# Kernel optimization log

Hardware: AMD Instinct MI355X
Metric: run time of the kernel (lower is better)

The kernel has to match this reference:

```python
import jax, jax.numpy as jnp
import numpy as np
from jax import lax

B, N, C, T = 8, 2000, 32, 12
K, F_CHEV, F_TIME = 3, 64, 64
LN_EPS = 1e-5


def setup_inputs() -> dict:
    key = jax.random.key(0)
    ks = jax.random.split(key, 20)
    s = 0.1
    return {
        "x": jax.random.normal(ks[0], (B, N, C, T), jnp.float32),
        "cheb_polys": jax.random.normal(ks[1], (K, N, N), jnp.float32) * 0.02,
        # temporal attention params
        "U1": jax.random.normal(ks[2], (N,), jnp.float32) * s,
        "U2": jax.random.normal(ks[3], (C, N), jnp.float32) * s,
        "U3": jax.random.normal(ks[4], (C,), jnp.float32) * s,
        "be": jax.random.normal(ks[5], (1, T, T), jnp.float32) * s,
        "Ve": jax.random.normal(ks[6], (T, T), jnp.float32) * s,
        # spatial attention params
        "W1": jax.random.normal(ks[7], (T,), jnp.float32) * s,
        "W2": jax.random.normal(ks[8], (C, T), jnp.float32) * s,
        "W3": jax.random.normal(ks[9], (C,), jnp.float32) * s,
        "bs": jax.random.normal(ks[10], (1, N, N), jnp.float32) * s,
        "Vs": jax.random.normal(ks[11], (N, N), jnp.float32) * (s / np.sqrt(N)),
        # Chebyshev conv params, stacked (K, C, F_chev)
        "Theta": jax.random.normal(ks[12], (K, C, F_CHEV), jnp.float32) * (1.0 / np.sqrt(C)),
        # time conv (1x3) and residual conv (1x1), NCHW/OIHW layout
        "tc_w": jax.random.normal(ks[13], (F_TIME, F_CHEV, 1, 3), jnp.float32) * (1.0 / np.sqrt(3 * F_CHEV)),
        "tc_b": jnp.zeros((F_TIME,), jnp.float32),
        "rc_w": jax.random.normal(ks[14], (F_TIME, C, 1, 1), jnp.float32) * (1.0 / np.sqrt(C)),
        "rc_b": jnp.zeros((F_TIME,), jnp.float32),
        # LayerNorm over nb_time_filter
        "ln_g": jnp.ones((F_TIME,), jnp.float32),
        "ln_b": jnp.zeros((F_TIME,), jnp.float32),
    }


def _conv2d(x, w, b, stride_t):
    # x: (B, Cin, N, T), w: (Cout, Cin, kh, kw)
    pad_w = (w.shape[3] - 1) // 2
    y = lax.conv_general_dilated(
        x, w, window_strides=(1, stride_t),
        padding=[(0, 0), (pad_w, pad_w)],
        dimension_numbers=("NCHW", "OIHW", "NCHW"))
    return y + b[None, :, None, None]


def reference(x, cheb_polys, U1, U2, U3, be, Ve, W1, W2, W3, bs, Vs,
              Theta, tc_w, tc_b, rc_w, rc_b, ln_g, ln_b):
    b, n, c, t = x.shape

    # ---- temporal attention: (B, T, T) ----
    lhs = jnp.einsum("bnct,n->btc", x, U1)              # x.permute(0,3,2,1) @ U1
    lhs = jnp.einsum("btc,cn->btn", lhs, U2)
    rhs = jnp.einsum("c,bnct->bnt", U3, x)
    E = jnp.einsum("ij,bjk->bik", Ve,
                   jax.nn.sigmoid(jnp.einsum("btn,bnu->btu", lhs, rhs) + be))
    temporal_At = jax.nn.softmax(E, axis=1)             # (B, T, T)

    # apply temporal attention
    x_TAt = jnp.matmul(x.reshape(b, n * c, t), temporal_At).reshape(b, n, c, t)

    # ---- spatial attention on x_TAt: (B, N, N) ----
    lhs_s = jnp.einsum("bnct,t->bnc", x_TAt, W1)
    lhs_s = jnp.einsum("bnc,ct->bnt", lhs_s, W2)
    rhs_s = jnp.einsum("c,bnct->btn", W3, x_TAt)        # (W3 @ x).transpose(-1,-2)
    S = jnp.einsum("ij,bjk->bik", Vs,
                   jax.nn.sigmoid(jnp.einsum("bnt,btm->bnm", lhs_s, rhs_s) + bs))
    spatial_At = jax.nn.softmax(S, axis=1)              # (B, N, N)

    # ---- Chebyshev graph conv with spatial attention ----
    # A[b,k,j,i] = cheb[k,j,i] * SAt[b,j,i]; out = relu(sum_k A^T x Theta_k)
    A = cheb_polys[None, :, :, :] * spatial_At[:, None, :, :]   # (B, K, N, N)
    h = jnp.einsum("bkji,bjct->bkitc", A, x)                    # (B, K, N, T, C)
    spatial_gcn = jax.nn.relu(jnp.einsum("bkitc,kcf->bift", h, Theta))  # (B, N, F, T)

    # ---- temporal conv + residual + LayerNorm ----
    time_out = _conv2d(spatial_gcn.transpose(0, 2, 1, 3), tc_w, tc_b, 1)  # (B, F_time, N, T')
    x_res = _conv2d(x.transpose(0, 2, 1, 3), rc_w, rc_b, 1)               # (B, F_time, N, T')
    z = jax.nn.relu(x_res + time_out).transpose(0, 3, 2, 1)               # (B, T', N, F_time)

    mu = jnp.mean(z, axis=-1, keepdims=True)
    var = jnp.mean((z - mu) ** 2, axis=-1, keepdims=True)
    zn = (z - mu) * lax.rsqrt(var + LN_EPS) * ln_g + ln_b

    return zn.transpose(0, 2, 3, 1)                                       # (B, N, F_time, T')
```

## Files before the change

### kernel.cpp

```cpp
#include <hip/hip_runtime.h>
#include <hip/hip_bf16.h>
#include <math.h>

#define B_ 8
#define N_ 2000
#define C_ 32
#define T_ 12
#define K_ 3
#define FC_ 64
#define FT_ 64
#define PW 2048

typedef short bf16x8 __attribute__((ext_vector_type(8)));
typedef float f32x4 __attribute__((ext_vector_type(4)));

__device__ __forceinline__ float sigmoidf(float v) { return 1.0f / (1.0f + __expf(-v)); }
__device__ __forceinline__ float bf2f(unsigned short u) {
    union { unsigned int i; float f; } v; v.i = ((unsigned int)u) << 16; return v.f;
}
__device__ __forceinline__ unsigned short f2bf(float f) {
    union { __hip_bfloat16 h; unsigned short u; } v; v.h = __float2bfloat16(f); return v.u;
}
typedef const __attribute__((address_space(1))) void* gas_t;
typedef __attribute__((address_space(3))) void* las_t;
__device__ __forceinline__ void gload16(const unsigned short* g, unsigned short* l) {
    __builtin_amdgcn_global_load_lds((gas_t)g, (las_t)l, 16, 0, 0);
}

__global__ __launch_bounds__(256) void k_tprep(const float* __restrict__ x, const float* __restrict__ U1,
                                               const float* __restrict__ U3,
                                               float* __restrict__ rhsT, float* __restrict__ plh) {
    int b = blockIdx.y, chunk = blockIdx.x;
    int tid = threadIdx.x;
    int nl = tid >> 5, c = tid & 31;
    int w = tid >> 6;
    float u3 = U3[c];
    float plA[12];
#pragma unroll
    for (int t = 0; t < 12; ++t) plA[t] = 0.f;
    for (int it = 0; it < 5; ++it) {
        int n = chunk * 40 + it * 8 + nl;
        const float* xp = x + ((size_t)(b * 2000 + n) * 32 + c) * 12;
        float4 v0 = *(const float4*)xp, v1 = *(const float4*)(xp + 4), v2 = *(const float4*)(xp + 8);
        float xv[12] = {v0.x, v0.y, v0.z, v0.w, v1.x, v1.y, v1.z, v1.w, v2.x, v2.y, v2.z, v2.w};
        float rv[12];
#pragma unroll
        for (int t = 0; t < 12; ++t) rv[t] = u3 * xv[t];
#pragma unroll
        for (int off = 16; off >= 1; off >>= 1)
#pragma unroll
            for (int t = 0; t < 12; ++t) rv[t] += __shfl_xor(rv[t], off);
        if (c == 0) {
#pragma unroll
            for (int t = 0; t < 12; ++t) rhsT[(size_t)(b * 2000 + n) * 12 + t] = rv[t];
        }
        float u1 = U1[n];
#pragma unroll
        for (int t = 0; t < 12; ++t) plA[t] += u1 * xv[t];
    }
#pragma unroll
    for (int t = 0; t < 12; ++t) plA[t] += __shfl_xor(plA[t], 32);
    __shared__ float accs[4][32][12];
    if ((tid & 63) < 32) {
#pragma unroll
        for (int t = 0; t < 12; ++t) accs[w][c][t] = plA[t];
    }
    __syncthreads();
    if (tid < 384) {
        int c2 = tid / 12, t2 = tid % 12;
        float s = accs[0][c2][t2] + accs[1][c2][t2] + accs[2][c2][t2] + accs[3][c2][t2];
        plh[((size_t)(b * 50 + chunk)) * 384 + tid] = s;
    }
}

__global__ __launch_bounds__(256) void k_tred(const float* __restrict__ plh, float* __restrict__ lhs1) {
    int b = blockIdx.x;
    for (int q = threadIdx.x; q < 384; q += 256) {
        const float* p = plh + (size_t)b * 50 * 384 + q;
        float s = 0.f;
        for (int ch = 0; ch < 50; ++ch) s += p[(size_t)ch * 384];
        int c = q / 12, t = q % 12;
        lhs1[(b * 12 + t) * 32 + c] = s;
    }
}

__global__ __launch_bounds__(256) void k_lhsT(const float* __restrict__ lhs1, const float* __restrict__ U2,
                                              float* __restrict__ lhsT) {
    int gid = blockIdx.x * 256 + threadIdx.x;
    if (gid >= B_ * T_ * N_) return;
    int n = gid % N_;
    int bt = gid / N_;
    const float* l1 = lhs1 + bt * C_;
    float a = 0.f;
#pragma unroll
    for (int c = 0; c < C_; ++c) a += l1[c] * U2[c * N_ + n];
    lhsT[gid] = a;
}

__global__ __launch_bounds__(256) void k_tatt1(const float* __restrict__ lhsT, const float* __restrict__ rhsT,
                                               float* __restrict__ pP) {
    int b = blockIdx.y, ch = blockIdx.x;
    int tid = threadIdx.x;
    int n0 = ch * 125;
    __shared__ float sL[12][128];
    __shared__ float sR[128][12];
    for (int q = tid; q < 12 * 125; q += 256) {
        int t = q / 125, nn = q % 125;
        sL[t][nn] = lhsT[(size_t)(b * 12 + t) * 2000 + n0 + nn];
    }
    for (int q = tid; q < 125 * 12; q += 256) {
        int nn = q / 12, t = q % 12;
        sR[nn][t] = rhsT[(size_t)(b * 2000 + n0 + nn) * 12 + t];
    }
    __syncthreads();
    if (tid < 144) {
        int tP = tid / 12, uP = tid % 12;
        float a = 0.f;
#pragma unroll 5
        for (int nn = 0; nn < 125; ++nn) a += sL[tP][nn] * sR[nn][uP];
        pP[(size_t)(b * 16 + ch) * 144 + tid] = a;
    }
}

__global__ __launch_bounds__(256) void k_tatt2(const float* __restrict__ pP, const float* __restrict__ be,
                                               const float* __restrict__ Ve, float* __restrict__ At) {
    int b = blockIdx.x, tid = threadIdx.x;
    __shared__ float sp[144], sE[144], mk[12], sk[12];
    int tP = tid / 12, uP = tid % 12;
    if (tid < 144) {
        float a = 0.f;
#pragma unroll
        for (int ch = 0; ch < 16; ++ch) a += pP[(size_t)(b * 16 + ch) * 144 + tid];
        sp[tid] = sigmoidf(a + be[tid]);
    }
    __syncthreads();
    if (tid < 144) {
        float e = 0.f;
#pragma unroll
        for (int j = 0; j < 12; ++j) e += Ve[tP * 12 + j] * sp[j * 12 + uP];
        sE[tid] = e;
    }
    __syncthreads();
    if (tid < 12) {
        float m = -1e30f;
#pragma unroll
        for (int i = 0; i < 12; ++i) m = fmaxf(m, sE[i * 12 + tid]);
        float s = 0.f;
#pragma unroll
        for (int i = 0; i < 12; ++i) s += __expf(sE[i * 12 + tid] - m);
        mk[tid] = m; sk[tid] = 1.0f / s;
    }
    __syncthreads();
    if (tid < 144) At[b * 144 + tid] = __expf(sE[tid] - mk[uP]) * sk[uP];
}

__global__ __launch_bounds__(256) void k_xsp(const float* __restrict__ x, const float* __restrict__ At,
                                             const float* __restrict__ W1, const float* __restrict__ W2,
                                             const float* __restrict__ W3,
                                             float* __restrict__ lhs_s, float* __restrict__ rhs_s) {
    int b = blockIdx.y, chunk = blockIdx.x;
    int tid = threadIdx.x, nl = tid >> 5, c = tid & 31;
    int n = chunk * 8 + nl;
    __shared__ float atl[144];
    __shared__ float w2l[384];
    __shared__ float w1l[12];
    if (tid < 144) atl[tid] = At[b * 144 + tid];
    if (tid >= 144 && tid < 156) w1l[tid - 144] = W1[tid - 144];
    for (int q = tid; q < 384; q += 256) w2l[q] = W2[q];
    __syncthreads();
    const float* xp = x + ((size_t)(b * 2000 + n) * 32 + c) * 12;
    float4 v0 = *(const float4*)xp, v1 = *(const float4*)(xp + 4), v2 = *(const float4*)(xp + 8);
    float xv[12] = {v0.x, v0.y, v0.z, v0.w, v1.x, v1.y, v1.z, v1.w, v2.x, v2.y, v2.z, v2.w};
    float xa[12];
#pragma unroll
    for (int t = 0; t < 12; ++t) {
        float s = 0.f;
#pragma unroll
        for (int u = 0; u < 12; ++u) s += xv[u] * atl[u * 12 + t];
        xa[t] = s;
    }
    float w3 = W3[c];
    float rv[12], lv[12];
    float l1 = 0.f;
#pragma unroll
    for (int t = 0; t < 12; ++t) l1 += xa[t] * w1l[t];
#pragma unroll
    for (int t = 0; t < 12; ++t) { rv[t] = w3 * xa[t]; lv[t] = l1 * w2l[c * 12 + t]; }
#pragma unroll
    for (int off = 16; off >= 1; off >>= 1)
#pragma unroll
        for (int t = 0; t < 12; ++t) { rv[t] += __shfl_xor(rv[t], off); lv[t] += __shfl_xor(lv[t], off); }
    if (c == 0) {
#pragma unroll
        for (int t = 0; t < 12; ++t) rhs_s[(size_t)(b * 12 + t) * 2000 + n] = rv[t];
#pragma unroll
        for (int t = 0; t < 12; ++t) lhs_s[(size_t)(b * 2000 + n) * 12 + t] = lv[t];
    }
}

__global__ __launch_bounds__(256) void k_wprep(const float* __restrict__ tc_w, const float* __restrict__ rc_w,
                                               float* __restrict__ tcwT, float* __restrict__ rcwT) {
    int gid = blockIdx.x * 256 + threadIdx.x;
    if (gid < 12288) {
        int fi = gid / 192, rem = gid % 192, f = rem / 3, d = rem % 3;
        tcwT[gid] = tc_w[(f * 64 + fi) * 3 + d];
    } else if (gid < 14336) {
        int q = gid - 12288;
        int c = q >> 6, f = q & 63;
        rcwT[q] = rc_w[f * 32 + c];
    }
}

__global__ __launch_bounds__(256) void k_vsb(const float* __restrict__ Vs, unsigned short* __restrict__ Vsb) {
    int gid = blockIdx.x * 256 + threadIdx.x;
    int row = gid >> 8, chunk = gid & 255;
    int p0 = chunk * 8;
    unsigned short o[8];
#pragma unroll
    for (int e = 0; e < 8; ++e) {
        int p = p0 + e;
        o[e] = (row < N_ && p < N_) ? f2bf(Vs[row * N_ + p]) : (unsigned short)0;
    }
    *(int4*)(Vsb + (size_t)row * PW + p0) = *(int4*)o;
}

__global__ __launch_bounds__(256) void k_chebT(const float* __restrict__ cheb, unsigned short* __restrict__ chebT) {
    int j0 = blockIdx.x * 64, i0 = blockIdx.y * 64, kk = blockIdx.z;
    __shared__ float Tl[64][65];
    int t = threadIdx.x;
    int rr = t >> 2, c0 = (t & 3) * 16;
    int j = j0 + rr;
#pragma unroll
    for (int e = 0; e < 16; ++e) {
        int i = i0 + c0 + e;
        Tl[rr][c0 + e] = (j < N_ && i < N_) ? cheb[(size_t)kk * 4000000 + (size_t)j * N_ + i] : 0.f;
    }
    __syncthreads();
    int l = t & 63, w = t >> 6;
    unsigned short o[16];
#pragma unroll
    for (int e = 0; e < 16; ++e) o[e] = f2bf(Tl[w * 16 + e][l]);
    unsigned short* dst = chebT + (size_t)kk * PW * PW + (size_t)(i0 + l) * PW + j0 + w * 16;
    *(int4*)dst = *(int4*)o;
    *(int4*)(dst + 8) = *(int4*)(o + 8);
}

__global__ __launch_bounds__(256) void k_xT(const float* __restrict__ x, unsigned short* __restrict__ xT) {
    int j0 = blockIdx.x * 64, r0 = blockIdx.y * 64, b = blockIdx.z;
    __shared__ float Tl[64][65];
    int t = threadIdx.x;
    int rr = t >> 2, c0 = (t & 3) * 16;
    int j = j0 + rr;
#pragma unroll
    for (int e = 0; e < 16; ++e) {
        int r = r0 + c0 + e;
        Tl[rr][c0 + e] = (j < N_) ? x[(size_t)(b * N_ + j) * 384 + r] : 0.f;
    }
    __syncthreads();
    int l = t & 63, w = t >> 6;
    unsigned short o[16];
#pragma unroll
    for (int e = 0; e < 16; ++e) o[e] = f2bf(Tl[w * 16 + e][l]);
    unsigned short* dst = xT + (size_t)b * 384 * PW + (size_t)(r0 + l) * PW + j0 + w * 16;
    *(int4*)dst = *(int4*)o;
    *(int4*)(dst + 8) = *(int4*)(o + 8);
}

__global__ __launch_bounds__(256) void k_sig(const float* __restrict__ lhs_s, const float* __restrict__ rhs_s,
                                             const float* __restrict__ bs, unsigned short* __restrict__ sigT) {
    int p0 = blockIdx.x * 64, i0 = blockIdx.y * 64, b = blockIdx.z;
    __shared__ float sL[64][12];
    __shared__ float sR[12][64];
    __shared__ float bsl[64][65];
    int t = threadIdx.x;
    for (int q = t; q < 768; q += 256) {
        int pp = q / 12, tt = q % 12;
        int p = p0 + pp;
        sL[pp][tt] = (p < N_) ? lhs_s[(b * N_ + p) * 12 + tt] : 0.f;
    }
    for (int q = t; q < 768; q += 256) {
        int tt = q >> 6, ii = q & 63;
        int i = i0 + ii;
        sR[tt][ii] = (i < N_) ? rhs_s[b * (T_ * N_) + tt * N_ + i] : 0.f;
    }
    {
        int pp = t >> 2, c0 = (t & 3) * 16;
        int p = p0 + pp;
        if (p < N_ && i0 + c0 + 15 < N_) {
            const float* src = bs + (size_t)p * N_ + i0 + c0;
#pragma unroll
            for (int e = 0; e < 16; e += 4) *(float4*)&bsl[pp][c0 + e] = *(const float4*)(src + e);
        } else {
#pragma unroll
            for (int e = 0; e < 16; ++e) {
                int i = i0 + c0 + e;
                bsl[pp][c0 + e] = (p < N_ && i < N_) ? bs[(size_t)p * N_ + i] : 0.f;
            }
        }
    }
    __syncthreads();
    int ii = t & 63, w = t >> 6;
    int i = i0 + ii;
    unsigned short o[16];
#pragma unroll
    for (int e = 0; e < 16; ++e) {
        int pl = w * 16 + e;
        int p = p0 + pl;
        float v = 0.f;
        if (p < N_ && i < N_) {
            float d = bsl[pl][ii];
#pragma unroll
            for (int tt = 0; tt < 12; ++tt) d += sL[pl][tt] * sR[tt][ii];
            v = sigmoidf(d);
        }
        o[e] = f2bf(v);
    }
    unsigned short* dst = sigT + (size_t)b * PW * PW + (size_t)i * PW + p0 + w * 16;
    *(int4*)dst = *(int4*)o;
    *(int4*)(dst + 8) = *(int4*)(o + 8);
}

#define FR_(R) (((R) ^ ((R) >> 2)) & 3)
__global__ __launch_bounds__(512) void k_gemm_S_mfma(const unsigned short* __restrict__ Vsb,
                                                     const unsigned short* __restrict__ sigT,
                                                     unsigned short* __restrict__ ST) {
    int lid = blockIdx.x + (blockIdx.y << 3) + (blockIdx.z << 6);
    int swz = (lid & 7) * 64 + (lid >> 3);
    int j0 = (swz & 7) * 256;
    int i0 = ((swz >> 3) & 7) * 256;
    int b = swz >> 6;
    const unsigned short* Ap = sigT + (size_t)b * PW * PW;
    __shared__ unsigned short As[2][2][8192];
    __shared__ unsigned short Bs[2][2][8192];
    int t = threadIdx.x, lane = t & 63, w = t >> 6;
    int wr = w >> 2, wc = w & 3;
    int l15 = lane & 15, kseg = lane >> 4;
    f32x4 acc[8][4];
#pragma unroll
    for (int m = 0; m < 8; ++m)
#pragma unroll
        for (int n = 0; n < 4; ++n)
#pragma unroll
            for (int q = 0; q < 4; ++q) acc[m][n][q] = 0.f;
    int srow = t >> 2;
    int gchunk = ((t & 3) ^ FR_(srow)) * 8;
    const unsigned short* gA = Ap + (size_t)(i0 + srow) * PW + gchunk;
    const unsigned short* gB = Vsb + (size_t)(j0 + srow) * PW + gchunk;
    int ldw = w * 512;
#define SA_(buf_, kt_, kh_) do { \
    gload16(gA + (size_t)(kt_) * 64 + (kh_) * 32, &As[buf_][kh_][ldw]); \
    gload16(gA + (size_t)128 * PW + (size_t)(kt_) * 64 + (kh_) * 32, &As[buf_][kh_][4096 + ldw]); \
} while (0)
#define SB_(buf_, kt_, kh_) do { \
    gload16(gB + (size_t)(kt_) * 64 + (kh_) * 32, &Bs[buf_][kh_][ldw]); \
    gload16(gB + (size_t)128 * PW + (size_t)(kt_) * 64 + (kh_) * 32, &Bs[buf_][kh_][4096 + ldw]); \
} while (0)
#define RDA(kh_, buf_) { _Pragma("unroll") for (int m = 0; m < 8; ++m) { \
    int R = wr * 128 + m * 16 + l15; \
    aR[m] = *(const bf16x8*)&As[buf_][kh_][R * 32 + ((kseg ^ FR_(R)) << 3)]; } }
#define RDB(kh_, nh_, buf_) { _Pragma("unroll") for (int n = 0; n < 2; ++n) { \
    int R = wc * 64 + (nh_) * 32 + n * 16 + l15; \
    bR[n] = *(const bf16x8*)&Bs[buf_][kh_][R * 32 + ((kseg ^ FR_(R)) << 3)]; } }
#define LGKM0 do { asm volatile("s_waitcnt lgkmcnt(0)" ::: "memory"); __builtin_amdgcn_sched_barrier(0); } while (0)
#define MMA(nh_) do { __builtin_amdgcn_s_setprio(1); \
    _Pragma("unroll") for (int m = 0; m < 8; ++m) \
    _Pragma("unroll") for (int n = 0; n < 2; ++n) \
        acc[m][(nh_) * 2 + n] = __builtin_amdgcn_mfma_f32_16x16x32_bf16(aR[m], bR[n], acc[m][(nh_) * 2 + n], 0, 0, 0); \
    __builtin_amdgcn_s_setprio(0); } while (0)
    SA_(0, 0, 0); SB_(0, 0, 0); SA_(0, 0, 1); SB_(0, 0, 1);
    SA_(1, 1, 0); SB_(1, 1, 0);
    asm volatile("s_waitcnt vmcnt(4)" ::: "memory");
    __builtin_amdgcn_s_barrier();
    for (int kt = 0; kt < 32; ++kt) {
        int cur = kt & 1, nb = cur ^ 1;
        bf16x8 aR[8], bR[2];
        RDA(0, cur); RDB(0, 0, cur);
        if (kt + 1 < 32) SA_(nb, kt + 1, 1);
        __builtin_amdgcn_s_barrier();
        LGKM0;
        MMA(0);
        __builtin_amdgcn_s_barrier();
        RDB(0, 1, cur);
        if (kt + 1 < 32) SB_(nb, kt + 1, 1);
        __builtin_amdgcn_s_barrier();
        LGKM0;
        MMA(1);
        __builtin_amdgcn_s_barrier();
        RDA(1, cur); RDB(1, 0, cur);
        if (kt + 2 < 32) SA_(cur, kt + 2, 0);
        __builtin_amdgcn_s_barrier();
        LGKM0;
        MMA(0);
        __builtin_amdgcn_s_barrier();
        RDB(1, 1, cur);
        if (kt + 2 < 32) SB_(cur, kt + 2, 0);
        __builtin_amdgcn_s_barrier();
        LGKM0;
        MMA(1);
        if (kt < 30) asm volatile("s_waitcnt vmcnt(4)" ::: "memory");
        else         asm volatile("s_waitcnt vmcnt(0)" ::: "memory");
        __builtin_amdgcn_s_barrier();
    }
#undef SA_
#undef SB_
#undef RDA
#undef RDB
#undef LGKM0
#undef MMA
    unsigned short* Sp = ST + (size_t)b * PW * PW;
#pragma unroll
    for (int m = 0; m < 8; ++m) {
        int row0 = i0 + wr * 128 + m * 16 + (kseg << 2);
#pragma unroll
        for (int n = 0; n < 4; ++n) {
            int col = j0 + wc * 64 + (n >> 1) * 32 + (n & 1) * 16 + l15;
#pragma unroll
            for (int q = 0; q < 4; ++q)
                Sp[(size_t)(row0 + q) * PW + col] = f2bf(acc[m][n][q]);
        }
    }
}

__global__ __launch_bounds__(256) void k_smrow(const unsigned short* __restrict__ ST,
                                               float* __restrict__ gm, float* __restrict__ gs) {
    int wid = threadIdx.x >> 6, lane = threadIdx.x & 63;
    int b = blockIdx.y;
    int i = blockIdx.x * 4 + wid;
    const unsigned short* rp = ST + (size_t)b * PW * PW + (size_t)i * PW;
    float vals[32];
    float m = -1e30f;
#pragma unroll
    for (int k = 0; k < 4; ++k) {
        int j0 = lane * 8 + k * 512;
        if (j0 < N_) {
            union { int4 v; unsigned short s[8]; } u;
            u.v = *(const int4*)(rp + j0);
#pragma unroll
            for (int e = 0; e < 8; ++e) {
                vals[k * 8 + e] = bf2f(u.s[e]);
                m = fmaxf(m, vals[k * 8 + e]);
            }
        } else {
#pragma unroll
            for (int e = 0; e < 8; ++e) vals[k * 8 + e] = -1e30f;
        }
    }
#pragma unroll
    for (int off = 32; off >= 1; off >>= 1) m = fmaxf(m, __shfl_xor(m, off));
    float s = 0.f;
#pragma unroll
    for (int k = 0; k < 32; ++k) s += __expf(vals[k] - m);
#pragma unroll
    for (int off = 32; off >= 1; off >>= 1) s += __shfl_xor(s, off);
    if (lane == 0) {
        gm[b * 2048 + i] = m;
        gs[b * 2048 + i] = 1.0f / s;
    }
}

__global__ __launch_bounds__(512) void k_gemm_cheb_mfma(const unsigned short* __restrict__ chebT,
                                                        const unsigned short* __restrict__ ST,
                                                        const float* __restrict__ gm, const float* __restrict__ gs,
                                                        const unsigned short* __restrict__ xT,
                                                        unsigned short* __restrict__ h2) {
    int bk = blockIdx.y;
    int b = bk / 3, kk = bk % 3;
    int i0 = blockIdx.x * 128;
    const unsigned short* Ac = chebT + (size_t)kk * PW * PW;
    const unsigned short* Sa = ST + (size_t)b * PW * PW;
    const unsigned short* Bx = xT + (size_t)b * 384 * PW;
    __shared__ unsigned short As[2][2][4096];
    __shared__ unsigned short Bs[2][2][12288];
    int t = threadIdx.x, lane = t & 63, w = t >> 6;
    int wr = w >> 2, wc = w & 3;
    int l15 = lane & 15, kseg = lane >> 4;
    f32x4 acc[4][6];
#pragma unroll
    for (int a = 0; a < 4; ++a)
#pragma unroll
        for (int c = 0; c < 6; ++c)
#pragma unroll
            for (int q = 0; q < 4; ++q) acc[a][c][q] = 0.f;
    int arow = t >> 2, achk = t & 3;
    const unsigned short* gac = Ac + (size_t)(i0 + arow) * PW + achk * 8;
    const unsigned short* gsa = Sa + (size_t)(i0 + arow) * PW + achk * 8;
    float gmv = gm[b * 2048 + i0 + arow];
    float gsv = gs[b * 2048 + i0 + arow];
    int awoff = arow * 32 + ((achk ^ FR_(arow)) << 3);
    int brow = t >> 2;
    int bchk = ((t & 3) ^ FR_(brow)) * 8;
    const unsigned short* gB = Bx + (size_t)brow * PW + bchk;
    int ldw = w * 512;
    union U8 { int4 v; unsigned short s[8]; };
#define SB_(buf_, kt_, kh_) do { \
    gload16(gB + (size_t)(kt_) * 64 + (kh_) * 32, &Bs[buf_][kh_][ldw]); \
    gload16(gB + (size_t)128 * PW + (size_t)(kt_) * 64 + (kh_) * 32, &Bs[buf_][kh_][4096 + ldw]); \
    gload16(gB + (size_t)256 * PW + (size_t)(kt_) * 64 + (kh_) * 32, &Bs[buf_][kh_][8192 + ldw]); \
} while (0)
#define WRA(buf_, kh_, cc, ss) do { U8 o_; \
    _Pragma("unroll") for (int e = 0; e < 8; ++e) \
        o_.s[e] = f2bf(bf2f((cc).s[e]) * __expf(bf2f((ss).s[e]) - gmv) * gsv); \
    *(int4*)&As[buf_][kh_][awoff] = o_.v; } while (0)
#define RDA(kh_, buf_) { _Pragma("unroll") for (int m = 0; m < 4; ++m) { \
    int R = wr * 64 + m * 16 + l15; \
    aR[m] = *(const bf16x8*)&As[buf_][kh_][R * 32 + ((kseg ^ FR_(R)) << 3)]; } }
#define RDB(kh_, nh_, buf_) { _Pragma("unroll") for (int n = 0; n < 3; ++n) { \
    int R = wc * 96 + (nh_) * 48 + n * 16 + l15; \
    bR[n] = *(const bf16x8*)&Bs[buf_][kh_][R * 32 + ((kseg ^ FR_(R)) << 3)]; } }
#define LGKM0 do { asm volatile("s_waitcnt lgkmcnt(0)" ::: "memory"); __builtin_amdgcn_sched_barrier(0); } while (0)
#define BAR __builtin_amdgcn_s_barrier()
#define MMA(nh_) do { __builtin_amdgcn_s_setprio(1); \
    _Pragma("unroll") for (int m = 0; m < 4; ++m) \
    _Pragma("unroll") for (int n = 0; n < 3; ++n) \
        acc[m][(nh_) * 3 + n] = __builtin_amdgcn_mfma_f32_16x16x32_bf16(aR[m], bR[n], acc[m][(nh_) * 3 + n], 0, 0, 0); \
    __builtin_amdgcn_s_setprio(0); } while (0)
    {
        U8 cc, ss;
        cc.v = *(const int4*)(gac);      ss.v = *(const int4*)(gsa);      WRA(0, 0, cc, ss);
        cc.v = *(const int4*)(gac + 32); ss.v = *(const int4*)(gsa + 32); WRA(0, 1, cc, ss);
        cc.v = *(const int4*)(gac + 64); ss.v = *(const int4*)(gsa + 64); WRA(1, 0, cc, ss);
        cc.v = *(const int4*)(gac + 96); ss.v = *(const int4*)(gsa + 96); WRA(1, 1, cc, ss);
    }
    SB_(0, 0, 0); SB_(0, 0, 1); SB_(1, 1, 0); SB_(1, 1, 1);
    asm volatile("s_waitcnt vmcnt(0) lgkmcnt(0)" ::: "memory");
    BAR;
    for (int kt = 0; kt < 32; ++kt) {
        int cur = kt & 1;
        bf16x8 aR[4], bR[3];
        U8 ca0, sa0, ca1, sa1;
        bool pf = (kt + 2 < 32);
        RDA(0, cur); RDB(0, 0, cur);
        if (pf) { ca0.v = *(const int4*)(gac + (size_t)(kt + 2) * 64); sa0.v = *(const int4*)(gsa + (size_t)(kt + 2) * 64); }
        BAR; LGKM0; MMA(0); BAR;
        RDB(0, 1, cur);
        if (pf) { ca1.v = *(const int4*)(gac + (size_t)(kt + 2) * 64 + 32); sa1.v = *(const int4*)(gsa + (size_t)(kt + 2) * 64 + 32); }
        BAR; LGKM0; MMA(1); BAR;
        RDA(1, cur); RDB(1, 0, cur);
        if (pf) { WRA(cur, 0, ca0, sa0); SB_(cur, kt + 2, 0); }
        BAR; LGKM0; MMA(0); BAR;
        RDB(1, 1, cur);
        if (pf) { WRA(cur, 1, ca1, sa1); SB_(cur, kt + 2, 1); }
        BAR; LGKM0; MMA(1); BAR;
    }
#undef SB_
#undef WRA
#undef RDA
#undef RDB
#undef LGKM0
#undef BAR
#undef MMA
    unsigned short* hp = h2 + (size_t)bk * 768000;
#pragma unroll
    for (int fm = 0; fm < 4; ++fm) {
        int row0 = i0 + wr * 64 + fm * 16 + (kseg << 2);
#pragma unroll
        for (int fn = 0; fn < 6; ++fn) {
            int col = wc * 96 + fn * 16 + l15;
#pragma unroll
            for (int q = 0; q < 4; ++q) {
                int row = row0 + q;
                if (row < N_) hp[(size_t)row * 384 + col] = f2bf(acc[fm][fn][q]);
            }
        }
    }
}

__global__ __launch_bounds__(512) void k_final3(const float* __restrict__ x, const unsigned short* __restrict__ h2,
                                                const float* __restrict__ ThetaG,
                                                const float* __restrict__ tcwT, const float* __restrict__ tc_b,
                                                const float* __restrict__ rcwT, const float* __restrict__ rc_b,
                                                const float* __restrict__ ln_g, const float* __restrict__ ln_b,
                                                float* __restrict__ out) {
    __shared__ __align__(16) char smem[110848];
    unsigned int* gl = (unsigned int*)smem;
    unsigned short* th = (unsigned short*)(smem + 98560);
    float* red_s = (float*)(smem + 98560);
    float* red_q = red_s + 64 * 13;

    int tid = threadIdx.x;
    int n_l = tid & 63, fg = tid >> 6;
    int b = blockIdx.y;
    int node = blockIdx.x * 64 + n_l;
    bool ok = node < N_;
    int nd = ok ? node : N_ - 1;

    for (int q = tid; q < 6144; q += 512) th[q] = f2bf(ThetaG[q]);
    __syncthreads();

    float acc[8][12];
#pragma unroll
    for (int ff = 0; ff < 8; ++ff)
#pragma unroll
        for (int t = 0; t < 12; ++t) acc[ff][t] = 0.f;
    const unsigned short* hb = h2 + (size_t)b * 3 * 768000 + (size_t)nd * 384;
#pragma unroll
    for (int kk = 0; kk < 3; ++kk) {
        const unsigned short* hp = hb + (size_t)kk * 768000;
#pragma unroll 2
        for (int c = 0; c < 32; ++c) {
            const unsigned short* hq = hp + c * 12;
            uint2 u0 = *(const uint2*)(hq);
            uint2 u1 = *(const uint2*)(hq + 4);
            uint2 u2 = *(const uint2*)(hq + 8);
            float h[12];
            h[0] = bf2f((unsigned short)u0.x);  h[1] = bf2f((unsigned short)(u0.x >> 16));
            h[2] = bf2f((unsigned short)u0.y);  h[3] = bf2f((unsigned short)(u0.y >> 16));
            h[4] = bf2f((unsigned short)u1.x);  h[5] = bf2f((unsigned short)(u1.x >> 16));
            h[6] = bf2f((unsigned short)u1.y);  h[7] = bf2f((unsigned short)(u1.y >> 16));
            h[8] = bf2f((unsigned short)u2.x);  h[9] = bf2f((unsigned short)(u2.x >> 16));
            h[10] = bf2f((unsigned short)u2.y); h[11] = bf2f((unsigned short)(u2.y >> 16));
            const unsigned short* wv = th + (kk * 32 + c) * 64 + fg * 8;
            uint2 w01 = *(const uint2*)wv;
            uint2 w23 = *(const uint2*)(wv + 4);
            float wf[8];
            wf[0] = bf2f((unsigned short)w01.x); wf[1] = bf2f((unsigned short)(w01.x >> 16));
            wf[2] = bf2f((unsigned short)w01.y); wf[3] = bf2f((unsigned short)(w01.y >> 16));
            wf[4] = bf2f((unsigned short)w23.x); wf[5] = bf2f((unsigned short)(w23.x >> 16));
            wf[6] = bf2f((unsigned short)w23.y); wf[7] = bf2f((unsigned short)(w23.y >> 16));
#pragma unroll
            for (int ff = 0; ff < 8; ++ff)
#pragma unroll
                for (int t = 0; t < 12; ++t) acc[ff][t] = fmaf(h[t], wf[ff], acc[ff][t]);
        }
    }
    unsigned int* gr = gl + n_l * 385 + fg * 48;
#pragma unroll
    for (int ff = 0; ff < 8; ++ff)
#pragma unroll
        for (int tp = 0; tp < 6; ++tp) {
            float a0 = fmaxf(acc[ff][2 * tp], 0.f), a1 = fmaxf(acc[ff][2 * tp + 1], 0.f);
            gr[ff * 6 + tp] = (unsigned int)f2bf(a0) | ((unsigned int)f2bf(a1) << 16);
        }
    __syncthreads();

    float z[8][12];
#pragma unroll
    for (int ff = 0; ff < 8; ++ff) {
        float bias = tc_b[fg * 8 + ff] + rc_b[fg * 8 + ff];
#pragma unroll
        for (int t = 0; t < 12; ++t) z[ff][t] = bias;
    }
    const float* xp = x + (size_t)(b * 2000 + nd) * 384;
#pragma unroll 2
    for (int c = 0; c < 32; ++c) {
        float4 x0 = *(const float4*)(xp + c * 12);
        float4 x1 = *(const float4*)(xp + c * 12 + 4);
        float4 x2 = *(const float4*)(xp + c * 12 + 8);
        float xv[12] = {x0.x, x0.y, x0.z, x0.w, x1.x, x1.y, x1.z, x1.w, x2.x, x2.y, x2.z, x2.w};
        float4 r0 = *(const float4*)(rcwT + c * 64 + fg * 8);
        float4 r1 = *(const float4*)(rcwT + c * 64 + fg * 8 + 4);
        float rw[8] = {r0.x, r0.y, r0.z, r0.w, r1.x, r1.y, r1.z, r1.w};
#pragma unroll
        for (int ff = 0; ff < 8; ++ff)
#pragma unroll
            for (int t = 0; t < 12; ++t) z[ff][t] = fmaf(xv[t], rw[ff], z[ff][t]);
    }
    const unsigned int* grow = gl + n_l * 385;
    for (int fi = 0; fi < 64; ++fi) {
        float g[12];
#pragma unroll
        for (int j = 0; j < 6; ++j) {
            unsigned int u = grow[fi * 6 + j];
            g[2 * j] = bf2f((unsigned short)u);
            g[2 * j + 1] = bf2f((unsigned short)(u >> 16));
        }
        const float* wp = tcwT + (fi * 64 + fg * 8) * 3;
        float4 w0 = *(const float4*)(wp);
        float4 w1 = *(const float4*)(wp + 4);
        float4 w2 = *(const float4*)(wp + 8);
        float4 w3 = *(const float4*)(wp + 12);
        float4 w4 = *(const float4*)(wp + 16);
        float4 w5 = *(const float4*)(wp + 20);
        float wb[24] = {w0.x, w0.y, w0.z, w0.w, w1.x, w1.y, w1.z, w1.w,
                        w2.x, w2.y, w2.z, w2.w, w3.x, w3.y, w3.z, w3.w,
                        w4.x, w4.y, w4.z, w4.w, w5.x, w5.y, w5.z, w5.w};
#pragma unroll
        for (int ff = 0; ff < 8; ++ff) {
            float a0 = wb[ff * 3], a1 = wb[ff * 3 + 1], a2 = wb[ff * 3 + 2];
            z[ff][0] = fmaf(g[0], a1, fmaf(g[1], a2, z[ff][0]));
#pragma unroll
            for (int t = 1; t < 11; ++t)
                z[ff][t] = fmaf(g[t - 1], a0, fmaf(g[t], a1, fmaf(g[t + 1], a2, z[ff][t])));
            z[ff][11] = fmaf(g[10], a0, fmaf(g[11], a1, z[ff][11]));
        }
    }
#pragma unroll
    for (int ff = 0; ff < 8; ++ff)
#pragma unroll
        for (int t = 0; t < 12; ++t) z[ff][t] = fmaxf(z[ff][t], 0.f);

    float s[12], q[12];
#pragma unroll
    for (int t = 0; t < 12; ++t) { s[t] = 0.f; q[t] = 0.f; }
#pragma unroll
    for (int ff = 0; ff < 8; ++ff)
#pragma unroll
        for (int t = 0; t < 12; ++t) { s[t] += z[ff][t]; q[t] += z[ff][t] * z[ff][t]; }
    __syncthreads();
    for (int g = 0; g < 8; ++g) {
        if (fg == g) {
            if (g == 0) {
#pragma unroll
                for (int t = 0; t < 12; ++t) { red_s[n_l * 13 + t] = s[t]; red_q[n_l * 13 + t] = q[t]; }
            } else {
#pragma unroll
                for (int t = 0; t < 12; ++t) { red_s[n_l * 13 + t] += s[t]; red_q[n_l * 13 + t] += q[t]; }
            }
        }
        __syncthreads();
    }
    float mu[12], rs[12];
#pragma unroll
    for (int t = 0; t < 12; ++t) {
        float m = red_s[n_l * 13 + t] * (1.0f / 64.0f);
        float v = red_q[n_l * 13 + t] * (1.0f / 64.0f) - m * m;
        mu[t] = m;
        rs[t] = rsqrtf(v + 1e-5f);
    }
    if (ok) {
        float* op = out + ((size_t)(b * 2000 + node) * 64 + fg * 8) * 12;
#pragma unroll
        for (int ff = 0; ff < 8; ++ff) {
            float lg = ln_g[fg * 8 + ff], lb = ln_b[fg * 8 + ff];
            float o[12];
#pragma unroll
            for (int t = 0; t < 12; ++t) o[t] = (z[ff][t] - mu[t]) * rs[t] * lg + lb;
#pragma unroll
            for (int tq = 0; tq < 3; ++tq)
                *(float4*)(op + ff * 12 + tq * 4) = make_float4(o[tq * 4], o[tq * 4 + 1], o[tq * 4 + 2], o[tq * 4 + 3]);
        }
    }
}

extern "C" void kernel_launch(void* const* d_in, const int* in_sizes, int n_in,
                              void* d_out, int out_size, void* d_ws, size_t ws_size,
                              hipStream_t stream) {
    const float* x     = (const float*)d_in[0];
    const float* cheb  = (const float*)d_in[1];
    const float* U1    = (const float*)d_in[2];
    const float* U2    = (const float*)d_in[3];
    const float* U3    = (const float*)d_in[4];
    const float* be    = (const float*)d_in[5];
    const float* Ve    = (const float*)d_in[6];
    const float* W1    = (const float*)d_in[7];
    const float* W2    = (const float*)d_in[8];
    const float* W3    = (const float*)d_in[9];
    const float* bs    = (const float*)d_in[10];
    const float* Vs    = (const float*)d_in[11];
    const float* Theta = (const float*)d_in[12];
    const float* tc_w  = (const float*)d_in[13];
    const float* tc_b  = (const float*)d_in[14];
    const float* rc_w  = (const float*)d_in[15];
    const float* rc_b  = (const float*)d_in[16];
    const float* ln_g  = (const float*)d_in[17];
    const float* ln_b  = (const float*)d_in[18];
    float* out = (float*)d_out;

    float* ws    = (float*)d_ws;
    float* At    = ws;
    float* lhs1  = ws + 1152;
    float* lhsT  = ws + 4224;
    float* rhsT  = ws + 196224;
    float* lhs_s = ws + 388224;
    float* rhs_s = ws + 580224;
    float* gm    = ws + 772224;
    float* gs    = ws + 788608;
    float* tcwT  = ws + 804992;
    float* rcwT  = ws + 817280;
    float* plh   = ws + 819328;
    float* pP    = ws + 972928;
    unsigned short* Vsb   = (unsigned short*)(ws + 991360);
    unsigned short* chebT = (unsigned short*)(ws + 3088512);
    unsigned short* xT    = (unsigned short*)(ws + 9379968);
    unsigned short* sigT  = (unsigned short*)(ws + 12525696);
    unsigned short* h2    = sigT;
    unsigned short* STb   = (unsigned short*)(ws + 29302912);

    k_wprep<<<56, 256, 0, stream>>>(tc_w, rc_w, tcwT, rcwT);
    k_vsb<<<2048, 256, 0, stream>>>(Vs, Vsb);
    k_chebT<<<dim3(32, 32, 3), 256, 0, stream>>>(cheb, chebT);
    k_xT<<<dim3(32, 6, 8), 256, 0, stream>>>(x, xT);
    k_tprep<<<dim3(50, 8), 256, 0, stream>>>(x, U1, U3, rhsT, plh);
    k_tred<<<8, 256, 0, stream>>>(plh, lhs1);
    k_lhsT<<<750, 256, 0, stream>>>(lhs1, U2, lhsT);
    k_tatt1<<<dim3(16, 8), 256, 0, stream>>>(lhsT, rhsT, pP);
    k_tatt2<<<8, 256, 0, stream>>>(pP, be, Ve, At);
    k_xsp<<<dim3(250, 8), 256, 0, stream>>>(x, At, W1, W2, W3, lhs_s, rhs_s);
    k_sig<<<dim3(32, 32, 8), 256, 0, stream>>>(lhs_s, rhs_s, bs, sigT);
    k_gemm_S_mfma<<<dim3(8, 8, 8), 512, 0, stream>>>(Vsb, sigT, STb);
    k_smrow<<<dim3(512, 8), 256, 0, stream>>>(STb, gm, gs);
    k_gemm_cheb_mfma<<<dim3(16, 24), 512, 0, stream>>>(chebT, STb, gm, gs, xT, h2);
    k_final3<<<dim3(32, 8), 512, 0, stream>>>(x, h2, Theta, tcwT, tc_b, rcwT, rc_b, ln_g, ln_b, out);
}
```

Measured before the change: 602.3 us.

## Restructure GEMM main loops to two barriers per k-step with wider MFMA phases

Both MFMA GEMM kernels (the spatial-score GEMM and the attention-weighted Chebyshev GEMM) change their main loop from four sub-phases per k-tile, each fenced by two barriers, to two phases per k-tile with one barrier each. Every phase now loads all B fragments (4 or 6 columns) and issues the full MFMA block. Global prefetches for the next half-tiles are issued alongside the LDS reads and waited on with vmcnt counts. This is meant to cut barrier and synchronisation overhead and give longer uninterrupted MFMA bursts. The cost is more live fragment registers, and the new prefetch/wait ordering needs to stay race-free.

```diff
diff --git a/kernel.cpp b/kernel.cpp
--- a/kernel.cpp
+++ b/kernel.cpp
@@ -358,48 +358,37 @@
 #define RDA(kh_, buf_) { _Pragma("unroll") for (int m = 0; m < 8; ++m) { \
     int R = wr * 128 + m * 16 + l15; \
     aR[m] = *(const bf16x8*)&As[buf_][kh_][R * 32 + ((kseg ^ FR_(R)) << 3)]; } }
-#define RDB(kh_, nh_, buf_) { _Pragma("unroll") for (int n = 0; n < 2; ++n) { \
-    int R = wc * 64 + (nh_) * 32 + n * 16 + l15; \
+#define RDB(kh_, buf_) { _Pragma("unroll") for (int n = 0; n < 4; ++n) { \
+    int R = wc * 64 + n * 16 + l15; \
     bR[n] = *(const bf16x8*)&Bs[buf_][kh_][R * 32 + ((kseg ^ FR_(R)) << 3)]; } }
 #define LGKM0 do { asm volatile("s_waitcnt lgkmcnt(0)" ::: "memory"); __builtin_amdgcn_sched_barrier(0); } while (0)
-#define MMA(nh_) do { __builtin_amdgcn_s_setprio(1); \
+#define MMA() do { __builtin_amdgcn_s_setprio(1); \
     _Pragma("unroll") for (int m = 0; m < 8; ++m) \
-    _Pragma("unroll") for (int n = 0; n < 2; ++n) \
-        acc[m][(nh_) * 2 + n] = __builtin_amdgcn_mfma_f32_16x16x32_bf16(aR[m], bR[n], acc[m][(nh_) * 2 + n], 0, 0, 0); \
+    _Pragma("unroll") for (int n = 0; n < 4; ++n) \
+        acc[m][n] = __builtin_amdgcn_mfma_f32_16x16x32_bf16(aR[m], bR[n], acc[m][n], 0, 0, 0); \
     __builtin_amdgcn_s_setprio(0); } while (0)
-    SA_(0, 0, 0); SB_(0, 0, 0); SA_(0, 0, 1); SB_(0, 0, 1);
+    SA_(0, 0, 0); SB_(0, 0, 0);
+    SA_(0, 0, 1); SB_(0, 0, 1);
     SA_(1, 1, 0); SB_(1, 1, 0);
-    asm volatile("s_waitcnt vmcnt(4)" ::: "memory");
-    __builtin_amdgcn_s_barrier();
     for (int kt = 0; kt < 32; ++kt) {
         int cur = kt & 1, nb = cur ^ 1;
-        bf16x8 aR[8], bR[2];
-        RDA(0, cur); RDB(0, 0, cur);
-        if (kt + 1 < 32) SA_(nb, kt + 1, 1);
+        bf16x8 aR[8], bR[4];
+        if (kt < 31) asm volatile("s_waitcnt vmcnt(8)" ::: "memory");
+        else         asm volatile("s_waitcnt vmcnt(4)" ::: "memory");
         __builtin_amdgcn_s_barrier();
+        __builtin_amdgcn_sched_barrier(0);
+        RDA(0, cur); RDB(0, cur);
+        if (kt + 1 < 32) { SA_(nb, kt + 1, 1); SB_(nb, kt + 1, 1); }
         LGKM0;
-        MMA(0);
-        __builtin_amdgcn_s_barrier();
-        RDB(0, 1, cur);
-        if (kt + 1 < 32) SB_(nb, kt + 1, 1);
-        __builtin_amdgcn_s_barrier();
-        LGKM0;
-        MMA(1);
-        __builtin_amdgcn_s_barrier();
-        RDA(1, cur); RDB(1, 0, cur);
-        if (kt + 2 < 32) SA_(cur, kt + 2, 0);
-        __builtin_amdgcn_s_barrier();
-        LGKM0;
-        MMA(0);
-        __builtin_amdgcn_s_barrier();
-        RDB(1, 1, cur);
-        if (kt + 2 < 32) SB_(cur, kt + 2, 0);
-        __builtin_amdgcn_s_barrier();
-        LGKM0;
-        MMA(1);
-        if (kt < 30) asm volatile("s_waitcnt vmcnt(4)" ::: "memory");
+        MMA();
+        if (kt < 31) asm volatile("s_waitcnt vmcnt(8)" ::: "memory");
         else         asm volatile("s_waitcnt vmcnt(0)" ::: "memory");
         __builtin_amdgcn_s_barrier();
+        __builtin_amdgcn_sched_barrier(0);
+        RDA(1, cur); RDB(1, cur);
+        if (kt + 2 < 32) { SA_(cur, kt + 2, 0); SB_(cur, kt + 2, 0); }
+        LGKM0;
+        MMA();
     }
 #undef SA_
 #undef SB_
@@ -413,7 +402,7 @@
         int row0 = i0 + wr * 128 + m * 16 + (kseg << 2);
 #pragma unroll
         for (int n = 0; n < 4; ++n) {
-            int col = j0 + wc * 64 + (n >> 1) * 32 + (n & 1) * 16 + l15;
+            int col = j0 + wc * 64 + n * 16 + l15;
 #pragma unroll
             for (int q = 0; q < 4; ++q)
                 Sp[(size_t)(row0 + q) * PW + col] = f2bf(acc[m][n][q]);
@@ -504,50 +493,58 @@
 #define RDA(kh_, buf_) { _Pragma("unroll") for (int m = 0; m < 4; ++m) { \
     int R = wr * 64 + m * 16 + l15; \
     aR[m] = *(const bf16x8*)&As[buf_][kh_][R * 32 + ((kseg ^ FR_(R)) << 3)]; } }
-#define RDB(kh_, nh_, buf_) { _Pragma("unroll") for (int n = 0; n < 3; ++n) { \
-    int R = wc * 96 + (nh_) * 48 + n * 16 + l15; \
+#define RDB(kh_, buf_) { _Pragma("unroll") for (int n = 0; n < 6; ++n) { \
+    int R = wc * 96 + n * 16 + l15; \
     bR[n] = *(const bf16x8*)&Bs[buf_][kh_][R * 32 + ((kseg ^ FR_(R)) << 3)]; } }
 #define LGKM0 do { asm volatile("s_waitcnt lgkmcnt(0)" ::: "memory"); __builtin_amdgcn_sched_barrier(0); } while (0)
-#define BAR __builtin_amdgcn_s_barrier()
-#define MMA(nh_) do { __builtin_amdgcn_s_setprio(1); \
+#define MMA() do { __builtin_amdgcn_s_setprio(1); \
     _Pragma("unroll") for (int m = 0; m < 4; ++m) \
-    _Pragma("unroll") for (int n = 0; n < 3; ++n) \
-        acc[m][(nh_) * 3 + n] = __builtin_amdgcn_mfma_f32_16x16x32_bf16(aR[m], bR[n], acc[m][(nh_) * 3 + n], 0, 0, 0); \
+    _Pragma("unroll") for (int n = 0; n < 6; ++n) \
+        acc[m][n] = __builtin_amdgcn_mfma_f32_16x16x32_bf16(aR[m], bR[n], acc[m][n], 0, 0, 0); \
     __builtin_amdgcn_s_setprio(0); } while (0)
+    U8 ca1, sa1;
     {
         U8 cc, ss;
+        SB_(0, 0, 0); SB_(0, 0, 1);
         cc.v = *(const int4*)(gac);      ss.v = *(const int4*)(gsa);      WRA(0, 0, cc, ss);
         cc.v = *(const int4*)(gac + 32); ss.v = *(const int4*)(gsa + 32); WRA(0, 1, cc, ss);
         cc.v = *(const int4*)(gac + 64); ss.v = *(const int4*)(gsa + 64); WRA(1, 0, cc, ss);
-        cc.v = *(const int4*)(gac + 96); ss.v = *(const int4*)(gsa + 96); WRA(1, 1, cc, ss);
-    }
-    SB_(0, 0, 0); SB_(0, 0, 1); SB_(1, 1, 0); SB_(1, 1, 1);
+        ca1.v = *(const int4*)(gac + 96); sa1.v = *(const int4*)(gsa + 96);
+    }
     asm volatile("s_waitcnt vmcnt(0) lgkmcnt(0)" ::: "memory");
-    BAR;
+    __builtin_amdgcn_s_barrier();
     for (int kt = 0; kt < 32; ++kt) {
-        int cur = kt & 1;
-        bf16x8 aR[4], bR[3];
-        U8 ca0, sa0, ca1, sa1;
-        bool pf = (kt + 2 < 32);
-        RDA(0, cur); RDB(0, 0, cur);
-        if (pf) { ca0.v = *(const int4*)(gac + (size_t)(kt + 2) * 64); sa0.v = *(const int4*)(gsa + (size_t)(kt + 2) * 64); }
-        BAR; LGKM0; MMA(0); BAR;
-        RDB(0, 1, cur);
-        if (pf) { ca1.v = *(const int4*)(gac + (size_t)(kt + 2) * 64 + 32); sa1.v = *(const int4*)(gsa + (size_t)(kt + 2) * 64 + 32); }
-        BAR; LGKM0; MMA(1); BAR;
-        RDA(1, cur); RDB(1, 0, cur);
-        if (pf) { WRA(cur, 0, ca0, sa0); SB_(cur, kt + 2, 0); }
-        BAR; LGKM0; MMA(0); BAR;
-        RDB(1, 1, cur);
-        if (pf) { WRA(cur, 1, ca1, sa1); SB_(cur, kt + 2, 1); }
-        BAR; LGKM0; MMA(1); BAR;
+        int cur = kt & 1, nb = cur ^ 1;
+        bf16x8 aR[4], bR[6];
+        U8 ca0, sa0, nca1, nsa1;
+        bool p1 = (kt + 1 < 32), p2 = (kt + 2 < 32);
+        RDA(0, cur); RDB(0, cur);
+        if (p1) {
+            SB_(nb, kt + 1, 0); SB_(nb, kt + 1, 1);
+            WRA(nb, 1, ca1, sa1);
+        }
+        if (p2) {
+            ca0.v = *(const int4*)(gac + (size_t)(kt + 2) * 64);
+            sa0.v = *(const int4*)(gsa + (size_t)(kt + 2) * 64);
+            nca1.v = *(const int4*)(gac + (size_t)(kt + 2) * 64 + 32);
+            nsa1.v = *(const int4*)(gsa + (size_t)(kt + 2) * 64 + 32);
+        }
+        LGKM0;
+        MMA();
+        __builtin_amdgcn_s_barrier();
+        __builtin_amdgcn_sched_barrier(0);
+        RDA(1, cur); RDB(1, cur);
+        if (p2) { WRA(cur, 0, ca0, sa0); ca1 = nca1; sa1 = nsa1; }
+        LGKM0;
+        MMA();
+        __builtin_amdgcn_s_barrier();
+        __builtin_amdgcn_sched_barrier(0);
     }
 #undef SB_
 #undef WRA
 #undef RDA
 #undef RDB
 #undef LGKM0
-#undef BAR
 #undef MMA
     unsigned short* hp = h2 + (size_t)bk * 768000;
 #pragma unroll
```

Result: no change. 595.9 us (-1.1%).
